# Kernel tuning notes

Measured on AMD Instinct MI355X. Metric: run time of the kernel, lower is better.

Reference implementation:

```python
import jax, jax.numpy as jnp
import numpy as np

K = 6            # kmer length
NF = 8192        # n_filters (> 4**K so kmer_params has shape (NF, 4, K))
M = 4 ** K       # 4096 kmers
B = 1024         # batch


def setup_inputs() -> dict:
    key = jax.random.key(0)
    k1, k2 = jax.random.split(key)
    freq = jax.random.uniform(k1, (B, M), dtype=jnp.float32)          # kmer frequencies (B, 4^k)
    kmer_params = jax.random.normal(k2, (NF, 4, K), dtype=jnp.float32)
    temperature = jnp.ones((1,), dtype=jnp.float32)
    # base-4 digits of arange(4^k), most-significant first == itertools.product order
    pos = 4 ** jnp.arange(K - 1, -1, -1)
    kmer_idcs = ((jnp.arange(M)[:, None] // pos[None, :]) % 4).astype(jnp.int32)  # (M, K)
    return {"freq": freq, "kmer_params": kmer_params,
            "temperature": temperature, "kmer_idcs": kmer_idcs}


def reference(freq, kmer_params, temperature, kmer_idcs):
    k = kmer_params.shape[-1]
    # matches[f, i] = sum_j kmer_params[f, kmer_idcs[i, j], j]
    # Advanced indexing broadcasts (M, k) indices against arange(k): result (F, M, k).
    # This replaces torch's expand-to-(F, M, 1, k) + gather + squeeze + sum(-1).
    matches = kmer_params[:, kmer_idcs, jnp.arange(k)].sum(axis=-1)   # (F, M)
    probs = jax.nn.softmax(matches / temperature, axis=1)             # softmax over kmers
    pooled = freq @ probs.T                                           # (B, F)
    profile = pooled / pooled.sum(axis=1, keepdims=True)
    return profile
```

## Files before the change

### kernel.cpp

```cpp
#include <hip/hip_runtime.h>


typedef __bf16  bf16x8 __attribute__((ext_vector_type(8)));
typedef float   f32x4  __attribute__((ext_vector_type(4)));

#define GLD16(gp, lp)                                                          \
  __builtin_amdgcn_global_load_lds(                                            \
      (const __attribute__((address_space(1))) void*)(gp),                     \
      (__attribute__((address_space(3))) void*)(lp), 16, 0, 0)

__device__ __forceinline__ short f2bf(float x) {
  unsigned u = __float_as_uint(x);
  unsigned r = (u + 0x7fffu + ((u >> 16) & 1u)) >> 16;
  return (short)r;
}

__device__ __forceinline__ float wave_max(float v) {
  #pragma unroll
  for (int off = 32; off; off >>= 1) v = fmaxf(v, __shfl_xor(v, off, 64));
  return v;
}
__device__ __forceinline__ float wave_sum(float v) {
  #pragma unroll
  for (int off = 32; off; off >>= 1) v += __shfl_xor(v, off, 64);
  return v;
}

__global__ __launch_bounds__(256) void prep_kernel(const float* __restrict__ freq,
                                                   short* __restrict__ freqb,
                                                   const float* __restrict__ kp,
                                                   const float* __restrict__ temp,
                                                   float* __restrict__ E1t,
                                                   float* __restrict__ E2) {
  if (blockIdx.x < 4096) {
    const int d = blockIdx.x;
    const int g = (d & 7) * 512 + (d >> 3);
    int idx = g * 256 + threadIdx.x;
    float4 v = ((const float4*)freq)[idx];
    short4 o;
    o.x = f2bf(v.x); o.y = f2bf(v.y); o.z = f2bf(v.z); o.w = f2bf(v.w);
    ((short4*)freqb)[idx] = o;
  } else {
    const int t = threadIdx.x;
    const int lane = t & 63, wave = t >> 6;
    const int f = (blockIdx.x - 4096) * 4 + wave;
    const float* P = kp + f * 24;
    const int d0 = (lane >> 4) & 3, d1 = (lane >> 2) & 3, d2 = lane & 3;
    const float thi = P[d0 * 6 + 0] + P[d1 * 6 + 1] + P[d2 * 6 + 2];
    const float tlo = P[d0 * 6 + 3] + P[d1 * 6 + 4] + P[d2 * 6 + 5];
    const float mxhi = wave_max(thi), mxlo = wave_max(tlo);
    const float invT = 1.0f / temp[0];
    const float e1 = __expf((thi - mxhi) * invT);
    const float e2 = __expf((tlo - mxlo) * invT);
    const float s1 = wave_sum(e1), s2 = wave_sum(e2);
    const float invZ = 1.0f / (s1 * s2);
    E1t[lane * 8192 + f] = e1 * invZ;
    E2[(size_t)f * 64 + lane] = e2;
  }
}

__global__ __launch_bounds__(256, 4) void gemm_kernel(const short* __restrict__ A,
                                                      const float* __restrict__ E1t,
                                                      const float* __restrict__ E2,
                                                      float* __restrict__ C) {
  __shared__ short As[3][64 * 64];

  const int t = threadIdx.x;
  const int lane = t & 63, wave = t >> 6;
  const int quad = lane >> 4, l16 = lane & 15;

  const int d  = blockIdx.y * 64 + blockIdx.x;
  const int L  = (d & 7) * 128 + (d >> 3);
  const int m0 = (L >> 6) * 64;
  const int n0 = (L & 63) * 128;
  const int wn = wave * 32;

  f32x4 acc[4][2];
  #pragma unroll
  for (int i = 0; i < 4; i++)
    #pragma unroll
    for (int j = 0; j < 2; j++) acc[i][j] = (f32x4){0.f, 0.f, 0.f, 0.f};

  int nrow[2];
  #pragma unroll
  for (int j = 0; j < 2; j++) nrow[j] = n0 + wn + j * 16 + l16;
  bf16x8 e2f[2][2];
  #pragma unroll
  for (int j = 0; j < 2; j++)
    #pragma unroll
    for (int ks = 0; ks < 2; ks++) {
      const float* p = E2 + (size_t)nrow[j] * 64 + (ks * 4 + quad) * 8;
      float4 lo = *(const float4*)p, hi = *(const float4*)(p + 4);
      bf16x8 bb;
      bb[0] = (__bf16)lo.x; bb[1] = (__bf16)lo.y;
      bb[2] = (__bf16)lo.z; bb[3] = (__bf16)lo.w;
      bb[4] = (__bf16)hi.x; bb[5] = (__bf16)hi.y;
      bb[6] = (__bf16)hi.z; bb[7] = (__bf16)hi.w;
      e2f[ks][j] = bb;
    }

  const int lane_row = lane >> 3;
  const int src_col = ((lane & 7) ^ lane_row) * 8;
  const int sw = l16 & 7;
  const int chunk = wave * 2;
  const short* Abase = A + (size_t)(m0 + lane_row) * 4096 + src_col;

  #define STG(kt, buf) do {                                                    \
    GLD16(Abase + (size_t)((chunk + 0) * 8) * 4096 + (kt) * 64,                \
          &As[buf][(chunk + 0) * 512 + lane * 8]);                             \
    GLD16(Abase + (size_t)((chunk + 1) * 8) * 4096 + (kt) * 64,                \
          &As[buf][(chunk + 1) * 512 + lane * 8]);                             \
  } while (0)

  STG(0, 0);
  float e1n[2], e1c[2];
  #pragma unroll
  for (int j = 0; j < 2; j++) e1n[j] = E1t[nrow[j]];
  STG(1, 1);

  const f32x4 Z4 = (f32x4){0.f, 0.f, 0.f, 0.f};

  #pragma unroll 1
  for (int kt = 0; kt < 64; ++kt) {
    const int cb = kt % 3;
    const int sb = (kt + 2) % 3;
    const int tn = (kt + 1 > 63) ? 63 : kt + 1;
    const int ts = (kt + 2 > 63) ? 63 : kt + 2;

    asm volatile("s_waitcnt vmcnt(4)" ::: "memory");
    __builtin_amdgcn_s_barrier();

    bf16x8 a[4][2];
    #pragma unroll
    for (int i = 0; i < 4; i++)
      #pragma unroll
      for (int ks = 0; ks < 2; ks++)
        a[i][ks] = *(const bf16x8*)&As[cb][(i * 16 + l16) * 64 +
                                          (((ks * 4 + quad) ^ sw) * 8)];

    #pragma unroll
    for (int j = 0; j < 2; j++) e1c[j] = e1n[j];
    #pragma unroll
    for (int j = 0; j < 2; j++) e1n[j] = E1t[tn * 8192 + nrow[j]];
    STG(ts, sb);

    __builtin_amdgcn_s_setprio(1);
    #pragma unroll
    for (int j = 0; j < 2; j++) {
      const f32x4 s4 = (f32x4){e1c[j], e1c[j], e1c[j], e1c[j]};
      #pragma unroll
      for (int i = 0; i < 4; i++) {
        f32x4 P = __builtin_amdgcn_mfma_f32_16x16x32_bf16(a[i][0], e2f[0][j], Z4, 0, 0, 0);
        P = __builtin_amdgcn_mfma_f32_16x16x32_bf16(a[i][1], e2f[1][j], P, 0, 0, 0);
        acc[i][j] += s4 * P;
      }
    }
    __builtin_amdgcn_s_setprio(0);
  }

  asm volatile("s_waitcnt vmcnt(0)" ::: "memory");

  #pragma unroll
  for (int i = 0; i < 4; i++) {
    #pragma unroll
    for (int r = 0; r < 4; r++) {
      const int brow = m0 + i * 16 + quad * 4 + r;
      float* crow = C + (size_t)brow * 8192 + n0 + wn + l16;
      #pragma unroll
      for (int j = 0; j < 2; j++) crow[j * 16] = acc[i][j][r];
    }
  }
  #undef STG
}

__global__ __launch_bounds__(256) void norm_kernel(float* __restrict__ out) {
  const int b = (blockIdx.x & 7) * 128 + (blockIdx.x >> 3);
  const int t = threadIdx.x;
  const int lane = t & 63, wave = t >> 6;
  __shared__ float red[4];

  float4* row = (float4*)(out + (size_t)b * 8192);
  float4 v[8];
  float s = 0.0f;
  #pragma unroll
  for (int q = 0; q < 8; q++) {
    v[q] = row[q * 256 + t];
    s += (v[q].x + v[q].y) + (v[q].z + v[q].w);
  }
  float ws = wave_sum(s);
  if (lane == 0) red[wave] = ws;
  __syncthreads();
  float tot = (red[0] + red[1]) + (red[2] + red[3]);
  float inv = 1.0f / tot;
  #pragma unroll
  for (int q = 0; q < 8; q++) {
    v[q].x *= inv; v[q].y *= inv; v[q].z *= inv; v[q].w *= inv;
    row[q * 256 + t] = v[q];
  }
}

extern "C" void kernel_launch(void* const* d_in, const int* in_sizes, int n_in,
                              void* d_out, int out_size, void* d_ws, size_t ws_size,
                              hipStream_t stream) {
  const float* freq    = (const float*)d_in[0];
  const float* kparams = (const float*)d_in[1];
  const float* temp    = (const float*)d_in[2];

  float* out = (float*)d_out;

  short* freqb = (short*)d_ws;
  float* E1t   = (float*)(freqb + (size_t)1024 * 4096);
  float* E2    = E1t + (size_t)64 * 8192;

  prep_kernel<<<6144, 256, 0, stream>>>(freq, freqb, kparams, temp, E1t, E2);
  gemm_kernel<<<dim3(64, 16), 256, 0, stream>>>(freqb, E1t, E2, out);
  norm_kernel<<<1024, 256, 0, stream>>>(out);
}
```

Baseline: 160.4 us.

## Switch GEMM to 32x32x16 MFMA with 2x2 wave tiling

Replaces the per-wave 64x32 tile computed with 16x16x32 bf16 MFMAs by a 2x2 wave layout where each wave computes 32x64 using 32x32x16 MFMAs, with four K-chunks per E1 scaling group. The aim is fewer LDS A-fragment reads per wave and fewer scale-accumulate vector ops per MFMA output. Larger MFMAs have higher per-instruction latency. The change also drops the XCD-aware block index remapping in the prep and norm kernels, which may change L2 locality.

```diff
diff --git a/kernel.cpp b/kernel.cpp
--- a/kernel.cpp
+++ b/kernel.cpp
@@ -3,6 +3,7 @@
 
 typedef __bf16  bf16x8 __attribute__((ext_vector_type(8)));
 typedef float   f32x4  __attribute__((ext_vector_type(4)));
+typedef float   f32x16 __attribute__((ext_vector_type(16)));
 
 #define GLD16(gp, lp)                                                          \
   __builtin_amdgcn_global_load_lds(                                            \
@@ -33,9 +34,7 @@
                                                    float* __restrict__ E1t,
                                                    float* __restrict__ E2) {
   if (blockIdx.x < 4096) {
-    const int d = blockIdx.x;
-    const int g = (d & 7) * 512 + (d >> 3);
-    int idx = g * 256 + threadIdx.x;
+    int idx = blockIdx.x * 256 + threadIdx.x;
     float4 v = ((const float4*)freq)[idx];
     short4 o;
     o.x = f2bf(v.x); o.y = f2bf(v.y); o.z = f2bf(v.z); o.w = f2bf(v.w);
@@ -67,41 +66,42 @@
 
   const int t = threadIdx.x;
   const int lane = t & 63, wave = t >> 6;
-  const int quad = lane >> 4, l16 = lane & 15;
+  const int l31 = lane & 31, l5 = lane >> 5;
 
   const int d  = blockIdx.y * 64 + blockIdx.x;
   const int L  = (d & 7) * 128 + (d >> 3);
   const int m0 = (L >> 6) * 64;
   const int n0 = (L & 63) * 128;
-  const int wn = wave * 32;
-
-  f32x4 acc[4][2];
-  #pragma unroll
-  for (int i = 0; i < 4; i++)
-    #pragma unroll
-    for (int j = 0; j < 2; j++) acc[i][j] = (f32x4){0.f, 0.f, 0.f, 0.f};
-
-  int nrow[2];
-  #pragma unroll
-  for (int j = 0; j < 2; j++) nrow[j] = n0 + wn + j * 16 + l16;
-  bf16x8 e2f[2][2];
-  #pragma unroll
-  for (int j = 0; j < 2; j++)
-    #pragma unroll
-    for (int ks = 0; ks < 2; ks++) {
-      const float* p = E2 + (size_t)nrow[j] * 64 + (ks * 4 + quad) * 8;
+  const int wm = (wave & 1) * 32;
+  const int wn = (wave >> 1) * 64;
+
+  f32x16 acc[2];
+  #pragma unroll
+  for (int nf = 0; nf < 2; nf++)
+    #pragma unroll
+    for (int x = 0; x < 16; x++) acc[nf][x] = 0.f;
+
+  int ncol[2];
+  #pragma unroll
+  for (int nf = 0; nf < 2; nf++) ncol[nf] = n0 + wn + nf * 32 + l31;
+  bf16x8 e2f[4][2];
+  #pragma unroll
+  for (int nf = 0; nf < 2; nf++)
+    #pragma unroll
+    for (int kc = 0; kc < 4; kc++) {
+      const float* p = E2 + (size_t)ncol[nf] * 64 + kc * 16 + l5 * 8;
       float4 lo = *(const float4*)p, hi = *(const float4*)(p + 4);
       bf16x8 bb;
       bb[0] = (__bf16)lo.x; bb[1] = (__bf16)lo.y;
       bb[2] = (__bf16)lo.z; bb[3] = (__bf16)lo.w;
       bb[4] = (__bf16)hi.x; bb[5] = (__bf16)hi.y;
       bb[6] = (__bf16)hi.z; bb[7] = (__bf16)hi.w;
-      e2f[ks][j] = bb;
+      e2f[kc][nf] = bb;
     }
 
   const int lane_row = lane >> 3;
   const int src_col = ((lane & 7) ^ lane_row) * 8;
-  const int sw = l16 & 7;
+  const int swA = l31 & 7;
   const int chunk = wave * 2;
   const short* Abase = A + (size_t)(m0 + lane_row) * 4096 + src_col;
 
@@ -115,10 +115,8 @@
   STG(0, 0);
   float e1n[2], e1c[2];
   #pragma unroll
-  for (int j = 0; j < 2; j++) e1n[j] = E1t[nrow[j]];
+  for (int nf = 0; nf < 2; nf++) e1n[nf] = E1t[ncol[nf]];
   STG(1, 1);
-
-  const f32x4 Z4 = (f32x4){0.f, 0.f, 0.f, 0.f};
 
   #pragma unroll 1
   for (int kt = 0; kt < 64; ++kt) {
@@ -130,30 +128,30 @@
     asm volatile("s_waitcnt vmcnt(4)" ::: "memory");
     __builtin_amdgcn_s_barrier();
 
-    bf16x8 a[4][2];
-    #pragma unroll
-    for (int i = 0; i < 4; i++)
+    bf16x8 a[4];
+    #pragma unroll
+    for (int kc = 0; kc < 4; kc++)
+      a[kc] = *(const bf16x8*)&As[cb][(wm + l31) * 64 +
+                                      (((kc * 2 + l5) ^ swA) * 8)];
+
+    #pragma unroll
+    for (int nf = 0; nf < 2; nf++) e1c[nf] = e1n[nf];
+    #pragma unroll
+    for (int nf = 0; nf < 2; nf++) e1n[nf] = E1t[tn * 8192 + ncol[nf]];
+    STG(ts, sb);
+
+    __builtin_amdgcn_s_setprio(1);
+    #pragma unroll
+    for (int nf = 0; nf < 2; nf++) {
+      f32x16 P;
       #pragma unroll
-      for (int ks = 0; ks < 2; ks++)
-        a[i][ks] = *(const bf16x8*)&As[cb][(i * 16 + l16) * 64 +
-                                          (((ks * 4 + quad) ^ sw) * 8)];
-
-    #pragma unroll
-    for (int j = 0; j < 2; j++) e1c[j] = e1n[j];
-    #pragma unroll
-    for (int j = 0; j < 2; j++) e1n[j] = E1t[tn * 8192 + nrow[j]];
-    STG(ts, sb);
-
-    __builtin_amdgcn_s_setprio(1);
-    #pragma unroll
-    for (int j = 0; j < 2; j++) {
-      const f32x4 s4 = (f32x4){e1c[j], e1c[j], e1c[j], e1c[j]};
+      for (int x = 0; x < 16; x++) P[x] = 0.f;
       #pragma unroll
-      for (int i = 0; i < 4; i++) {
-        f32x4 P = __builtin_amdgcn_mfma_f32_16x16x32_bf16(a[i][0], e2f[0][j], Z4, 0, 0, 0);
-        P = __builtin_amdgcn_mfma_f32_16x16x32_bf16(a[i][1], e2f[1][j], P, 0, 0, 0);
-        acc[i][j] += s4 * P;
-      }
+      for (int kc = 0; kc < 4; kc++)
+        P = __builtin_amdgcn_mfma_f32_32x32x16_bf16(a[kc], e2f[kc][nf], P, 0, 0, 0);
+      const float s = e1c[nf];
+      #pragma unroll
+      for (int x = 0; x < 16; x++) acc[nf][x] += s * P[x];
     }
     __builtin_amdgcn_s_setprio(0);
   }
@@ -161,20 +159,18 @@
   asm volatile("s_waitcnt vmcnt(0)" ::: "memory");
 
   #pragma unroll
-  for (int i = 0; i < 4; i++) {
-    #pragma unroll
-    for (int r = 0; r < 4; r++) {
-      const int brow = m0 + i * 16 + quad * 4 + r;
-      float* crow = C + (size_t)brow * 8192 + n0 + wn + l16;
-      #pragma unroll
-      for (int j = 0; j < 2; j++) crow[j * 16] = acc[i][j][r];
+  for (int nf = 0; nf < 2; nf++) {
+    #pragma unroll
+    for (int r = 0; r < 16; r++) {
+      const int brow = m0 + wm + (r & 3) + 8 * (r >> 2) + 4 * l5;
+      C[(size_t)brow * 8192 + ncol[nf]] = acc[nf][r];
     }
   }
   #undef STG
 }
 
 __global__ __launch_bounds__(256) void norm_kernel(float* __restrict__ out) {
-  const int b = (blockIdx.x & 7) * 128 + (blockIdx.x >> 3);
+  const int b = blockIdx.x;
   const int t = threadIdx.x;
   const int lane = t & 63, wave = t >> 6;
   __shared__ float red[4];
```

Result: no change. 163.0 us (+1.7%).
